# Kernel tuning notes

Measured on AMD Instinct MI355X. Metric: run time of the kernel, lower is better.

The kernel has to match this reference:

```python
import jax, jax.numpy as jnp
import numpy as np

B, N, C = 2, 2048, 1024
H = 16
D = C // H  # head_dim = 64
SCALE = D ** -0.5


def setup_inputs() -> dict:
    key = jax.random.key(0)
    k1, k2, k3, k4 = jax.random.split(key, 4)
    x = jax.random.normal(k1, (B, N, C), dtype=jnp.float32)
    # nn.Linear(in_dim, 3*out_dim, bias=False): store as [in, 3*out] for x @ W
    w_qkv = jax.random.normal(k2, (C, 3 * C), dtype=jnp.float32) * (C ** -0.5)
    w_proj = jax.random.normal(k3, (C, C), dtype=jnp.float32) * (C ** -0.5)
    b_proj = jax.random.normal(k4, (C,), dtype=jnp.float32) * 0.01
    return {"x": x, "w_qkv": w_qkv, "w_proj": w_proj, "b_proj": b_proj}


def reference(x, w_qkv, w_proj, b_proj):
    b, n, c = x.shape
    # QKV projection -> [3, B, H, N, D]
    qkv = (x @ w_qkv).reshape(b, n, 3, H, D).transpose(2, 0, 3, 1, 4)
    q, k, v = qkv[0], qkv[1], qkv[2]
    # scaled dot-product attention, full [B, H, N, N] scores as in original
    attn = jax.nn.softmax(jnp.einsum('bhqd,bhkd->bhqk', q * SCALE, k), axis=-1)
    out = jnp.einsum('bhqk,bhkd->bhqd', attn, v)  # [B, H, N, D]
    out = out.transpose(0, 2, 1, 3).reshape(b, n, c)
    return out @ w_proj + b_proj
```

## Files before the change

kernel.cpp:

```cpp
#include <hip/hip_runtime.h>

typedef unsigned short u16;
typedef float f32x4 __attribute__((ext_vector_type(4)));
typedef short bf16x8 __attribute__((ext_vector_type(8)));
typedef u16 u16x4 __attribute__((ext_vector_type(4)));
typedef u16 u16x8 __attribute__((ext_vector_type(8)));
typedef __bf16 bfr4 __attribute__((ext_vector_type(4)));

#define BB 2
#define NN 2048
#define CC 1024
#define HH 16
#define DD 64
#define MM (BB * NN)
#define NQKV (3 * CC)
#define QSCALE 0.18033688011112042f

#if __has_builtin(__builtin_amdgcn_exp2f)
#define EXP2(x) __builtin_amdgcn_exp2f(x)
#else
#define EXP2(x) exp2f(x)
#endif

__device__ __forceinline__ u16 f2bf(float f) {
    unsigned u = __float_as_uint(f);
    u += 0x7FFFu + ((u >> 16) & 1u);
    return (u16)(u >> 16);
}

__device__ __forceinline__ void ld_lds16(const u16* g, u16* l) {
    __builtin_amdgcn_global_load_lds(
        (const __attribute__((address_space(1))) unsigned int*)g,
        (__attribute__((address_space(3))) unsigned int*)l, 16, 0, 0);
}

__global__ __launch_bounds__(256) void k_prep(const float* __restrict__ x,
                                              const float* __restrict__ wqkv,
                                              const float* __restrict__ wproj,
                                              u16* __restrict__ Xb,
                                              u16* __restrict__ Wq,
                                              u16* __restrict__ Wp) {
    __shared__ float tile[64][65];
    int bid = blockIdx.x, t = threadIdx.x;
    if (bid < 2048) {
        int i = (bid * 256 + t) * 8;
        float4 a = *(const float4*)(x + i);
        float4 b = *(const float4*)(x + i + 4);
        u16x8 o;
        o[0] = f2bf(a.x); o[1] = f2bf(a.y); o[2] = f2bf(a.z); o[3] = f2bf(a.w);
        o[4] = f2bf(b.x); o[5] = f2bf(b.y); o[6] = f2bf(b.z); o[7] = f2bf(b.w);
        *(u16x8*)(Xb + i) = o;
        return;
    }
    const float* in;
    u16* out;
    int Nn, n0, k0;
    if (bid < 2048 + 768) {
        int b2 = bid - 2048;
        in = wqkv; out = Wq; Nn = NQKV;
        n0 = (b2 % 48) * 64; k0 = (b2 / 48) * 64;
    } else {
        int b3 = bid - 2816;
        in = wproj; out = Wp; Nn = CC;
        n0 = (b3 & 15) * 64; k0 = (b3 >> 4) * 64;
    }
    int tx = t & 63, ty = t >> 6;
#pragma unroll
    for (int r = 0; r < 64; r += 4)
        tile[ty + r][tx] = in[(size_t)(k0 + ty + r) * Nn + n0 + tx];
    __syncthreads();
#pragma unroll
    for (int r = 0; r < 64; r += 4)
        out[(size_t)(n0 + ty + r) * CC + k0 + tx] = f2bf(tile[tx][ty + r]);
}

__global__ __launch_bounds__(512, 2) void k_gemmq(
    const u16* __restrict__ A, const u16* __restrict__ B,
    u16* __restrict__ Qb, u16* __restrict__ Kb, u16* __restrict__ Vb) {
    const int Kd = 1024;
    __shared__ __align__(16) u16 Ah0[256][64], Bh0[192][64];
    __shared__ __align__(16) u16 Ah1[256][64], Bh1[192][64];

    int t = threadIdx.x, wave = t >> 6, lane = t & 63;
    int quad = lane >> 4, l16 = lane & 15;
    int wr = wave >> 2, wc = wave & 3;

    int cid = blockIdx.y * 16 + blockIdx.x;
    int swz = (cid & 7) * 32 + (cid >> 3);
    int m0 = (swz >> 4) * 256, n0 = (swz & 15) * 192;

    int strow = wave * 8 + (lane >> 3);
    int stdst = (lane & 7) * 8;
    int stsrc = ((lane & 7) ^ (lane >> 3)) * 8;

    f32x4 acc[8][3];
#pragma unroll
    for (int i = 0; i < 8; i++)
#pragma unroll
        for (int j = 0; j < 3; j++) acc[i][j] = f32x4{0.f, 0.f, 0.f, 0.f};

    auto STAGE = [&](int k0, u16 (*Ad)[64], u16 (*Bd)[64]) {
#pragma unroll
        for (int i = 0; i < 4; i++) {
            int row = i * 64 + strow;
            ld_lds16(A + (size_t)(m0 + row) * Kd + k0 + stsrc, &Ad[row][stdst]);
        }
#pragma unroll
        for (int i = 0; i < 3; i++) {
            int row = i * 64 + strow;
            ld_lds16(B + (size_t)(n0 + row) * Kd + k0 + stsrc, &Bd[row][stdst]);
        }
    };
    auto COMPUTE = [&](u16 (*As)[64], u16 (*Bs)[64]) {
#pragma unroll
        for (int s = 0; s < 2; s++) {
            int pos = ((s * 4 + quad) ^ (l16 & 7)) * 8;
            bf16x8 af[8], bg[3];
#pragma unroll
            for (int m = 0; m < 8; m++)
                af[m] = *(const bf16x8*)&As[wr * 128 + m * 16 + l16][pos];
#pragma unroll
            for (int n = 0; n < 3; n++)
                bg[n] = *(const bf16x8*)&Bs[wc * 48 + n * 16 + l16][pos];
            __builtin_amdgcn_s_setprio(1);
#pragma unroll
            for (int m = 0; m < 8; m++)
#pragma unroll
                for (int n = 0; n < 3; n++)
                    acc[m][n] = __builtin_amdgcn_mfma_f32_16x16x32_bf16(
                        af[m], bg[n], acc[m][n], 0, 0, 0);
            __builtin_amdgcn_s_setprio(0);
        }
    };

    STAGE(0, Ah0, Bh0);
    __syncthreads();
    for (int k0 = 0; k0 < Kd; k0 += 128) {
        STAGE(k0 + 64, Ah1, Bh1);
        COMPUTE(Ah0, Bh0);
        __syncthreads();
        if (k0 + 128 < Kd) STAGE(k0 + 128, Ah0, Bh0);
        COMPUTE(Ah1, Bh1);
        __syncthreads();
    }

#pragma unroll
    for (int m = 0; m < 8; m++)
#pragma unroll
        for (int n = 0; n < 3; n++)
#pragma unroll
            for (int r = 0; r < 4; r++) {
                int grow = m0 + wr * 128 + m * 16 + quad * 4 + r;
                int gcol = n0 + wc * 48 + n * 16 + l16;
                float v = acc[m][n][r];
                int three = gcol >> 10, rem = gcol & 1023;
                int h = rem >> 6, d = rem & 63;
                int bb = grow >> 11, nn = grow & 2047;
                if (three == 0) {
                    Qb[((size_t)(bb * HH + h) * NN + nn) * DD + d] = f2bf(v * QSCALE);
                } else if (three == 1) {
                    Kb[((size_t)(bb * HH + h) * NN + nn) * DD + d] = f2bf(v);
                } else {
                    Vb[((size_t)(bb * HH + h) * DD + d) * NN + nn] = f2bf(v);
                }
            }
}

__global__ __launch_bounds__(256) void k_gemmp(
    const u16* __restrict__ A, const u16* __restrict__ B,
    const float* __restrict__ bias, float* __restrict__ Cout) {
    const int Kd = 1024;
    __shared__ __align__(16) u16 Ah[64][128];
    __shared__ __align__(16) u16 Bh[128][128];

    int t = threadIdx.x, wave = t >> 6, lane = t & 63;
    int quad = lane >> 4, l16 = lane & 15;
    int m0 = blockIdx.x * 64, n0 = blockIdx.y * 128;

    int strow = lane >> 4;
    int stdst = (lane & 15) * 8;

    f32x4 acc[4][2];
#pragma unroll
    for (int i = 0; i < 4; i++)
#pragma unroll
        for (int j = 0; j < 2; j++) acc[i][j] = f32x4{0.f, 0.f, 0.f, 0.f};

    auto STAGE = [&](int k0) {
#pragma unroll
        for (int i = 0; i < 4; i++) {
            int row = wave * 16 + i * 4 + strow;
            int src = ((lane & 15) ^ (row & 7)) * 8;
            ld_lds16(A + (size_t)(m0 + row) * Kd + k0 + src, &Ah[row & 63][0] + stdst);
        }
#pragma unroll
        for (int i = 0; i < 8; i++) {
            int row = wave * 32 + i * 4 + strow;
            int src = ((lane & 15) ^ (row & 7)) * 8;
            ld_lds16(B + (size_t)(n0 + row) * Kd + k0 + src, &Bh[row & 127][0] + stdst);
        }
    };
    auto COMPUTE = [&]() {
#pragma unroll
        for (int s = 0; s < 4; s++) {
            int pos = ((s * 4 + quad) ^ (l16 & 7)) * 8;
            bf16x8 af[4], bg[2];
#pragma unroll
            for (int m = 0; m < 4; m++)
                af[m] = *(const bf16x8*)&Ah[m * 16 + l16][pos];
#pragma unroll
            for (int n = 0; n < 2; n++)
                bg[n] = *(const bf16x8*)&Bh[wave * 32 + n * 16 + l16][pos];
            __builtin_amdgcn_s_setprio(1);
#pragma unroll
            for (int m = 0; m < 4; m++)
#pragma unroll
                for (int n = 0; n < 2; n++)
                    acc[m][n] = __builtin_amdgcn_mfma_f32_16x16x32_bf16(
                        af[m], bg[n], acc[m][n], 0, 0, 0);
            __builtin_amdgcn_s_setprio(0);
        }
    };

    for (int k0 = 0; k0 < Kd; k0 += 128) {
        __syncthreads();
        STAGE(k0);
        __syncthreads();
        COMPUTE();
    }

#pragma unroll
    for (int m = 0; m < 4; m++)
#pragma unroll
        for (int n = 0; n < 2; n++)
#pragma unroll
            for (int r = 0; r < 4; r++) {
                int grow = m0 + m * 16 + quad * 4 + r;
                int gcol = n0 + wave * 32 + n * 16 + l16;
                Cout[(size_t)grow * CC + gcol] = acc[m][n][r] + bias[gcol];
            }
}

__global__ __launch_bounds__(512) void k_attn(const u16* __restrict__ Qb,
                                              const u16* __restrict__ Kb,
                                              const u16* __restrict__ VbT,
                                              u16* __restrict__ Ob) {
    __shared__ __align__(16) u16 Ks0[64][64], Ks1[64][64];
    __shared__ __align__(16) u16 Vs0[64][64], Vs1[64][64];
    __shared__ __align__(16) u16 Ps[8][16][72];

    int t = threadIdx.x, wave = t >> 6, lane = t & 63;
    int quad = lane >> 4, l16 = lane & 15;
    int bh = blockIdx.x, q0 = blockIdx.y * 128;
    const size_t kbase = (size_t)bh * NN * DD;
    const size_t vbase = (size_t)bh * DD * NN;

    int qrow = q0 + wave * 16 + l16;
    bf16x8 qf0 = *(const bf16x8*)&Qb[kbase + (size_t)qrow * DD + quad * 8];
    bf16x8 qf1 = *(const bf16x8*)&Qb[kbase + (size_t)qrow * DD + 32 + quad * 8];

    f32x4 o[4];
#pragma unroll
    for (int i = 0; i < 4; i++) o[i] = f32x4{0.f, 0.f, 0.f, 0.f};
    f32x4 lrow = f32x4{0.f, 0.f, 0.f, 0.f};

    int stgrp = lane & 7;
    int stsrc = (stgrp ^ (lane >> 3)) * 8;
    int strow = wave * 8 + (lane >> 3);
    int cf0 = (quad ^ (l16 & 7)) * 8;
    int cf1 = ((4 + quad) ^ (l16 & 7)) * 8;

    auto STAGE = [&](int cc, u16 (*Kd_)[64], u16 (*Vd_)[64]) {
        ld_lds16(&Kb[kbase + (size_t)(cc * 64 + strow) * DD + stsrc],
                 &Kd_[strow][stgrp * 8]);
        ld_lds16(&VbT[vbase + (size_t)strow * NN + cc * 64 + stsrc],
                 &Vd_[strow][stgrp * 8]);
    };

    auto COMPUTE = [&](u16 (*Ksrc)[64], u16 (*Vsrc)[64]) {
        bf16x8 kf[4][2];
#pragma unroll
        for (int kt = 0; kt < 4; kt++) {
            kf[kt][0] = *(const bf16x8*)&Ksrc[kt * 16 + l16][cf0];
            kf[kt][1] = *(const bf16x8*)&Ksrc[kt * 16 + l16][cf1];
        }
        f32x4 s[4];
        __builtin_amdgcn_s_setprio(1);
#pragma unroll
        for (int kt = 0; kt < 4; kt++) {
            f32x4 z = f32x4{0.f, 0.f, 0.f, 0.f};
            z = __builtin_amdgcn_mfma_f32_16x16x32_bf16(kf[kt][0], qf0, z, 0, 0, 0);
            z = __builtin_amdgcn_mfma_f32_16x16x32_bf16(kf[kt][1], qf1, z, 0, 0, 0);
            s[kt] = z;
        }
        __builtin_amdgcn_s_setprio(0);
#pragma unroll
        for (int kt = 0; kt < 4; kt++) {
            bfr4 pk;
#pragma unroll
            for (int r = 0; r < 4; r++) {
                float e = EXP2(s[kt][r]);
                lrow[r] += e;
                pk[r] = (__bf16)e;
            }
            *(bfr4*)&Ps[wave][l16][kt * 16 + quad * 4] = pk;
        }
        __asm__ volatile("s_waitcnt lgkmcnt(0)" ::: "memory");
        bf16x8 pb0 = *(const bf16x8*)&Ps[wave][l16][quad * 8];
        bf16x8 pb1 = *(const bf16x8*)&Ps[wave][l16][32 + quad * 8];
        __builtin_amdgcn_s_setprio(1);
#pragma unroll
        for (int dt = 0; dt < 4; dt++) {
            bf16x8 vf0 = *(const bf16x8*)&Vsrc[dt * 16 + l16][cf0];
            bf16x8 vf1 = *(const bf16x8*)&Vsrc[dt * 16 + l16][cf1];
            o[dt] = __builtin_amdgcn_mfma_f32_16x16x32_bf16(vf0, pb0, o[dt], 0, 0, 0);
            o[dt] = __builtin_amdgcn_mfma_f32_16x16x32_bf16(vf1, pb1, o[dt], 0, 0, 0);
        }
        __builtin_amdgcn_s_setprio(0);
    };

    STAGE(0, Ks0, Vs0);
    __syncthreads();

    for (int c = 0; c < NN / 64; c += 2) {
        STAGE(c + 1, Ks1, Vs1);
        COMPUTE(Ks0, Vs0);
        __syncthreads();
        if (c + 2 < NN / 64) STAGE(c + 2, Ks0, Vs0);
        COMPUTE(Ks1, Vs1);
        __syncthreads();
    }

    int b = bh >> 4, h = bh & 15;
    float l = (lrow[0] + lrow[1]) + (lrow[2] + lrow[3]);
    l += __shfl_xor(l, 16, 64);
    l += __shfl_xor(l, 32, 64);
    float inv = 1.f / l;
    int grow = b * NN + q0 + wave * 16 + l16;
#pragma unroll
    for (int dt = 0; dt < 4; dt++) {
        u16x4 hv;
#pragma unroll
        for (int r = 0; r < 4; r++) hv[r] = f2bf(o[dt][r] * inv);
        int gcol = h * DD + dt * 16 + quad * 4;
        *(u16x4*)&Ob[(size_t)grow * CC + gcol] = hv;
    }
}

extern "C" void kernel_launch(void* const* d_in, const int* in_sizes, int n_in,
                              void* d_out, int out_size, void* d_ws, size_t ws_size,
                              hipStream_t stream) {
    const float* x      = (const float*)d_in[0];
    const float* w_qkv  = (const float*)d_in[1];
    const float* w_proj = (const float*)d_in[2];
    const float* b_proj = (const float*)d_in[3];
    float* out = (float*)d_out;

    u16* p = (u16*)d_ws;
    u16* Xb = p; p += (size_t)MM * CC;
    u16* Wq = p; p += (size_t)NQKV * CC;
    u16* Wp = p; p += (size_t)CC * CC;
    u16* Qb = p; p += (size_t)MM * CC;
    u16* Kb = p; p += (size_t)MM * CC;
    u16* Vb = p; p += (size_t)MM * CC;
    u16* Ob = p; p += (size_t)MM * CC;

    k_prep<<<2048 + 768 + 256, 256, 0, stream>>>(x, w_qkv, w_proj, Xb, Wq, Wp);
    k_gemmq<<<dim3(NQKV / 192, MM / 256), 512, 0, stream>>>(Xb, Wq, Qb, Kb, Vb);
    k_attn<<<dim3(BB * HH, NN / 128), 512, 0, stream>>>(Qb, Kb, Vb, Ob);
    k_gemmp<<<dim3(MM / 64, CC / 128), 256, 0, stream>>>(Ob, Wp, b_proj, out);
}
```

Baseline: 188.6 us.

## Process two 16-row query tiles per wave in attention to reuse K/V fragments

Each attention wave now computes 32 query rows (two 16-row sub-tiles) instead of 16, so every K and V fragment read from LDS feeds twice as many MFMAs. The block covers 256 queries, which halves the grid and the total K/V staging traffic. The cost is more accumulator and fragment registers per thread and fewer blocks in flight, which reduces occupancy and latency hiding.

```diff
diff --git a/kernel.cpp b/kernel.cpp
--- a/kernel.cpp
+++ b/kernel.cpp
@@ -247,22 +247,28 @@
                                               u16* __restrict__ Ob) {
     __shared__ __align__(16) u16 Ks0[64][64], Ks1[64][64];
     __shared__ __align__(16) u16 Vs0[64][64], Vs1[64][64];
-    __shared__ __align__(16) u16 Ps[8][16][72];
+    __shared__ __align__(16) u16 Ps[8][32][72];
 
     int t = threadIdx.x, wave = t >> 6, lane = t & 63;
     int quad = lane >> 4, l16 = lane & 15;
-    int bh = blockIdx.x, q0 = blockIdx.y * 128;
+    int bh = blockIdx.x, q0 = blockIdx.y * 256;
     const size_t kbase = (size_t)bh * NN * DD;
     const size_t vbase = (size_t)bh * DD * NN;
 
-    int qrow = q0 + wave * 16 + l16;
-    bf16x8 qf0 = *(const bf16x8*)&Qb[kbase + (size_t)qrow * DD + quad * 8];
-    bf16x8 qf1 = *(const bf16x8*)&Qb[kbase + (size_t)qrow * DD + 32 + quad * 8];
-
-    f32x4 o[4];
-#pragma unroll
-    for (int i = 0; i < 4; i++) o[i] = f32x4{0.f, 0.f, 0.f, 0.f};
-    f32x4 lrow = f32x4{0.f, 0.f, 0.f, 0.f};
+    bf16x8 qf[2][2];
+#pragma unroll
+    for (int qj = 0; qj < 2; qj++) {
+        int qrow = q0 + wave * 32 + qj * 16 + l16;
+        qf[qj][0] = *(const bf16x8*)&Qb[kbase + (size_t)qrow * DD + quad * 8];
+        qf[qj][1] = *(const bf16x8*)&Qb[kbase + (size_t)qrow * DD + 32 + quad * 8];
+    }
+
+    f32x4 o[2][4];
+#pragma unroll
+    for (int qj = 0; qj < 2; qj++)
+#pragma unroll
+        for (int i = 0; i < 4; i++) o[qj][i] = f32x4{0.f, 0.f, 0.f, 0.f};
+    f32x4 lrow[2] = {f32x4{0.f, 0.f, 0.f, 0.f}, f32x4{0.f, 0.f, 0.f, 0.f}};
 
     int stgrp = lane & 7;
     int stsrc = (stgrp ^ (lane >> 3)) * 8;
@@ -284,37 +290,47 @@
             kf[kt][0] = *(const bf16x8*)&Ksrc[kt * 16 + l16][cf0];
             kf[kt][1] = *(const bf16x8*)&Ksrc[kt * 16 + l16][cf1];
         }
-        f32x4 s[4];
-        __builtin_amdgcn_s_setprio(1);
-#pragma unroll
-        for (int kt = 0; kt < 4; kt++) {
-            f32x4 z = f32x4{0.f, 0.f, 0.f, 0.f};
-            z = __builtin_amdgcn_mfma_f32_16x16x32_bf16(kf[kt][0], qf0, z, 0, 0, 0);
-            z = __builtin_amdgcn_mfma_f32_16x16x32_bf16(kf[kt][1], qf1, z, 0, 0, 0);
-            s[kt] = z;
-        }
-        __builtin_amdgcn_s_setprio(0);
-#pragma unroll
-        for (int kt = 0; kt < 4; kt++) {
-            bfr4 pk;
-#pragma unroll
-            for (int r = 0; r < 4; r++) {
-                float e = EXP2(s[kt][r]);
-                lrow[r] += e;
-                pk[r] = (__bf16)e;
-            }
-            *(bfr4*)&Ps[wave][l16][kt * 16 + quad * 4] = pk;
+#pragma unroll
+        for (int qj = 0; qj < 2; qj++) {
+            f32x4 s[4];
+            __builtin_amdgcn_s_setprio(1);
+#pragma unroll
+            for (int kt = 0; kt < 4; kt++) {
+                f32x4 z = f32x4{0.f, 0.f, 0.f, 0.f};
+                z = __builtin_amdgcn_mfma_f32_16x16x32_bf16(kf[kt][0], qf[qj][0], z, 0, 0, 0);
+                z = __builtin_amdgcn_mfma_f32_16x16x32_bf16(kf[kt][1], qf[qj][1], z, 0, 0, 0);
+                s[kt] = z;
+            }
+            __builtin_amdgcn_s_setprio(0);
+#pragma unroll
+            for (int kt = 0; kt < 4; kt++) {
+                bfr4 pk;
+#pragma unroll
+                for (int r = 0; r < 4; r++) {
+                    float e = EXP2(s[kt][r]);
+                    lrow[qj][r] += e;
+                    pk[r] = (__bf16)e;
+                }
+                *(bfr4*)&Ps[wave][qj * 16 + l16][kt * 16 + quad * 4] = pk;
+            }
         }
         __asm__ volatile("s_waitcnt lgkmcnt(0)" ::: "memory");
-        bf16x8 pb0 = *(const bf16x8*)&Ps[wave][l16][quad * 8];
-        bf16x8 pb1 = *(const bf16x8*)&Ps[wave][l16][32 + quad * 8];
+        bf16x8 pb[2][2];
+#pragma unroll
+        for (int qj = 0; qj < 2; qj++) {
+            pb[qj][0] = *(const bf16x8*)&Ps[wave][qj * 16 + l16][quad * 8];
+            pb[qj][1] = *(const bf16x8*)&Ps[wave][qj * 16 + l16][32 + quad * 8];
+        }
         __builtin_amdgcn_s_setprio(1);
 #pragma unroll
         for (int dt = 0; dt < 4; dt++) {
             bf16x8 vf0 = *(const bf16x8*)&Vsrc[dt * 16 + l16][cf0];
             bf16x8 vf1 = *(const bf16x8*)&Vsrc[dt * 16 + l16][cf1];
-            o[dt] = __builtin_amdgcn_mfma_f32_16x16x32_bf16(vf0, pb0, o[dt], 0, 0, 0);
-            o[dt] = __builtin_amdgcn_mfma_f32_16x16x32_bf16(vf1, pb1, o[dt], 0, 0, 0);
+#pragma unroll
+            for (int qj = 0; qj < 2; qj++) {
+                o[qj][dt] = __builtin_amdgcn_mfma_f32_16x16x32_bf16(vf0, pb[qj][0], o[qj][dt], 0, 0, 0);
+                o[qj][dt] = __builtin_amdgcn_mfma_f32_16x16x32_bf16(vf1, pb[qj][1], o[qj][dt], 0, 0, 0);
+            }
         }
         __builtin_amdgcn_s_setprio(0);
     };
@@ -332,18 +348,21 @@
     }
 
     int b = bh >> 4, h = bh & 15;
-    float l = (lrow[0] + lrow[1]) + (lrow[2] + lrow[3]);
-    l += __shfl_xor(l, 16, 64);
-    l += __shfl_xor(l, 32, 64);
-    float inv = 1.f / l;
-    int grow = b * NN + q0 + wave * 16 + l16;
-#pragma unroll
-    for (int dt = 0; dt < 4; dt++) {
-        u16x4 hv;
-#pragma unroll
-        for (int r = 0; r < 4; r++) hv[r] = f2bf(o[dt][r] * inv);
-        int gcol = h * DD + dt * 16 + quad * 4;
-        *(u16x4*)&Ob[(size_t)grow * CC + gcol] = hv;
+#pragma unroll
+    for (int qj = 0; qj < 2; qj++) {
+        float l = (lrow[qj][0] + lrow[qj][1]) + (lrow[qj][2] + lrow[qj][3]);
+        l += __shfl_xor(l, 16, 64);
+        l += __shfl_xor(l, 32, 64);
+        float inv = 1.f / l;
+        int grow = b * NN + q0 + wave * 32 + qj * 16 + l16;
+#pragma unroll
+        for (int dt = 0; dt < 4; dt++) {
+            u16x4 hv;
+#pragma unroll
+            for (int r = 0; r < 4; r++) hv[r] = f2bf(o[qj][dt][r] * inv);
+            int gcol = h * DD + dt * 16 + quad * 4;
+            *(u16x4*)&Ob[(size_t)grow * CC + gcol] = hv;
+        }
     }
 }
 
@@ -367,6 +386,6 @@
 
     k_prep<<<2048 + 768 + 256, 256, 0, stream>>>(x, w_qkv, w_proj, Xb, Wq, Wp);
     k_gemmq<<<dim3(NQKV / 192, MM / 256), 512, 0, stream>>>(Xb, Wq, Qb, Kb, Vb);
-    k_attn<<<dim3(BB * HH, NN / 128), 512, 0, stream>>>(Qb, Kb, Vb, Ob);
+    k_attn<<<dim3(BB * HH, NN / 256), 512, 0, stream>>>(Qb, Kb, Vb, Ob);
     k_gemmp<<<dim3(MM / 64, CC / 128), 256, 0, stream>>>(Ob, Wp, b_proj, out);
 }
```

Measured after the change: 184.8 us. 2.1% less time.
